# Kernel tuning notes

Hardware: AMD Instinct MI355X
Metric: run time of the kernel (lower is better)

## Reference

```python
import jax, jax.numpy as jnp
import numpy as np

B, N, D, K, NUM_CLASSES = 8, 2048, 256, 8, 32
BN_EPS = 1e-5


def l2norm(x):
    return x / jnp.maximum(jnp.linalg.norm(x, axis=-1, keepdims=True), 1e-12)


def mlp2(x, W1, b1, W2, b2):
    # get_mlp([3, 32, D]): Linear -> ReLU -> Linear -> ReLU
    return jax.nn.relu(jax.nn.relu(x @ W1 + b1) @ W2 + b2)


def bn(x, g, b):
    # training-mode BatchNorm1d over all edges (flattened leading dims)
    ax = tuple(range(x.ndim - 1))
    m = jnp.mean(x, axis=ax, keepdims=True)
    v = jnp.var(x, axis=ax, keepdims=True)
    return (x - m) * jax.lax.rsqrt(v + BN_EPS) * g + b


def setup_inputs() -> dict:
    key = jax.random.key(0)
    ks = jax.random.split(key, 24)
    p = lambda i, shape: jax.random.normal(ks[i], shape, jnp.float32) * 0.05
    class_table = p(0, (NUM_CLASSES, D)).at[0].set(0.0)  # padding_idx=0
    return dict(
        class_idx=jax.random.randint(ks[1], (B, N), 0, NUM_CLASSES),
        colors=jax.random.uniform(ks[2], (B, N, 3), jnp.float32),
        positions=jax.random.normal(ks[3], (B, N, 3), jnp.float32),
        class_table=class_table,
        pos_W1=p(4, (3, 32)), pos_b1=p(5, (32,)),
        pos_W2=p(6, (32, D)), pos_b2=p(7, (D,)),
        col_W1=p(8, (3, 32)), col_b1=p(9, (32,)),
        col_W2=p(10, (32, D)), col_b2=p(11, (D,)),
        merge_W=p(12, (3 * D, D)), merge_b=p(13, (D,)),
        g_W1=p(14, (2 * D, D)), g_b1=p(15, (D,)),
        g_g1=jnp.ones((D,), jnp.float32), g_be1=jnp.zeros((D,), jnp.float32),
        g_W2=p(16, (D, D)), g_b2=p(17, (D,)),
        g_g2=jnp.ones((D,), jnp.float32), g_be2=jnp.zeros((D,), jnp.float32),
        lin_W1=p(18, (D, D)), lin_b1=p(19, (D,)),
        lin_W2=p(20, (D, D)), lin_b2=p(21, (D,)),
    )


def reference(class_idx, colors, positions, class_table,
              pos_W1, pos_b1, pos_W2, pos_b2,
              col_W1, col_b1, col_W2, col_b2,
              merge_W, merge_b,
              g_W1, g_b1, g_g1, g_be1, g_W2, g_b2, g_g2, g_be2,
              lin_W1, lin_b1, lin_W2, lin_b2):
    # --- per-object feature embeddings, each L2-normalized ---
    ce = l2norm(class_table[class_idx])                                   # [B,N,D]
    col = l2norm(mlp2(colors, col_W1, col_b1, col_W2, col_b2))            # [B,N,D]
    pos = l2norm(mlp2(positions, pos_W1, pos_b1, pos_W2, pos_b2))         # [B,N,D]
    x = jax.nn.relu(jnp.concatenate([ce, col, pos], -1) @ merge_W + merge_b)  # [B,N,D]
    # --- dynamic kNN in feature space, per sample (self edge included) ---
    sq = jnp.sum(x * x, -1)                                               # [B,N]
    d = sq[:, :, None] + sq[:, None, :] - 2.0 * jnp.einsum('bid,bjd->bij', x, x)
    _, idx = jax.lax.top_k(-jax.lax.stop_gradient(d), K)                  # [B,N,K]
    xj = jax.vmap(lambda e, i: e[i])(x, idx)                              # [B,N,K,D]
    xi = jnp.broadcast_to(x[:, :, None, :], xj.shape)
    e = jnp.concatenate([xi, xj - xi], -1)                                # [B,N,K,2D]
    # --- edge MLP [2D,D,D] with BN, max aggregation over neighbors ---
    h = bn(jax.nn.relu(e @ g_W1 + g_b1), g_g1, g_be1)
    h = bn(jax.nn.relu(h @ g_W2 + g_b2), g_g2, g_be2)
    node = jnp.max(h, axis=2)                                             # [B,N,D]
    pooled = jnp.max(node, axis=1)                                        # global_max_pool -> [B,D]
    out = jax.nn.relu(jax.nn.relu(pooled @ lin_W1 + lin_b1) @ lin_W2 + lin_b2)
    return l2norm(out)
```

## Files before the change

### kernel.cpp

```cpp
#include <hip/hip_runtime.h>
#include <math.h>

#define BB 8
#define NN 2048
#define DD 256
#define KNN 8
#define NPTS (BB*NN)
#define NEDGE (NPTS*KNN)
#define BN_EPS 1e-5f
#define NSH 64
#define PSH 32

#define OFF_X      0
#define OFF_FEAT   (OFF_X + NPTS*DD)
#define OFF_STATS  (OFF_FEAT + NPTS*3*DD)
#define OFF_PMAXS  (OFF_STATS + NSH*1024)
#define OFF_SQ     (OFF_PMAXS + PSH*BB*DD)
#define OFF_PMINS  (OFF_SQ + NPTS)
#define OFF_IDX    (OFF_PMINS + PSH*BB*DD)
#define OFF_U      (OFF_IDX + NEDGE)
#define OFF_V      (OFF_U + NPTS*DD)
#define OFF_W2BF   (OFF_V + NPTS*DD)
#define OFF_BIASP  (OFF_W2BF + 32768)
#define OFF_XHI    (OFF_BIASP + DD)
#define OFF_XLO    (OFF_XHI + NPTS*DD/2)
#define OFF_MWH    (OFF_XLO + NPTS*DD/2)
#define OFF_MWL    (OFF_MWH + 98304)
#define OFF_WUH    (OFF_MWL + 98304)
#define OFF_WUL    (OFF_WUH + 32768)
#define OFF_WBH    (OFF_WUL + 32768)
#define OFF_WBL    (OFF_WBH + 32768)

typedef __attribute__((ext_vector_type(8))) short bf16x8;
typedef __attribute__((ext_vector_type(4))) float f32x4;

__device__ __forceinline__ unsigned short f2bf(float f) {
  unsigned int u = __float_as_uint(f);
  u += 0x7FFF + ((u >> 16) & 1);
  return (unsigned short)(u >> 16);
}
__device__ __forceinline__ float bf2f(unsigned short h) {
  return __uint_as_float((unsigned int)h << 16);
}

__global__ __launch_bounds__(256) void featurize(
    const int* __restrict__ cls, const float* __restrict__ colors, const float* __restrict__ positions,
    const float* __restrict__ ctab,
    const float* __restrict__ pW1, const float* __restrict__ pb1, const float* __restrict__ pW2, const float* __restrict__ pb2,
    const float* __restrict__ cW1, const float* __restrict__ cb1, const float* __restrict__ cW2, const float* __restrict__ cb2,
    unsigned short* __restrict__ feathi, unsigned short* __restrict__ featlo)
{
  __shared__ float wbuf[4][64];
  int tid = threadIdx.x;
  int wv = tid >> 6, lane = tid & 63;
  int p = blockIdx.x*4 + wv;
  if (lane < 32) {
    float c0 = colors[p*3+0], c1 = colors[p*3+1], c2 = colors[p*3+2];
    wbuf[wv][lane] = fmaxf(c0*cW1[lane] + c1*cW1[32+lane] + c2*cW1[64+lane] + cb1[lane], 0.f);
  } else {
    int l = lane - 32;
    float q0 = positions[p*3+0], q1 = positions[p*3+1], q2 = positions[p*3+2];
    wbuf[wv][32+l] = fmaxf(q0*pW1[l] + q1*pW1[32+l] + q2*pW1[64+l] + pb1[l], 0.f);
  }
  __syncthreads();
  int c = lane*4;
  float4 ce4 = *(const float4*)&ctab[(size_t)cls[p]*DD + c];
  float4 col4 = *(const float4*)&cb2[c];
  float4 pos4 = *(const float4*)&pb2[c];
  #pragma unroll
  for (int k = 0; k < 32; k++) {
    float ch = wbuf[wv][k], ph = wbuf[wv][32+k];
    float4 cw = *(const float4*)&cW2[k*DD + c];
    float4 pw = *(const float4*)&pW2[k*DD + c];
    col4.x += ch*cw.x; col4.y += ch*cw.y; col4.z += ch*cw.z; col4.w += ch*cw.w;
    pos4.x += ph*pw.x; pos4.y += ph*pw.y; pos4.z += ph*pw.z; pos4.w += ph*pw.w;
  }
  col4.x = fmaxf(col4.x, 0.f); col4.y = fmaxf(col4.y, 0.f);
  col4.z = fmaxf(col4.z, 0.f); col4.w = fmaxf(col4.w, 0.f);
  pos4.x = fmaxf(pos4.x, 0.f); pos4.y = fmaxf(pos4.y, 0.f);
  pos4.z = fmaxf(pos4.z, 0.f); pos4.w = fmaxf(pos4.w, 0.f);
  float sce  = ce4.x*ce4.x + ce4.y*ce4.y + ce4.z*ce4.z + ce4.w*ce4.w;
  float scol = col4.x*col4.x + col4.y*col4.y + col4.z*col4.z + col4.w*col4.w;
  float spos = pos4.x*pos4.x + pos4.y*pos4.y + pos4.z*pos4.z + pos4.w*pos4.w;
  #pragma unroll
  for (int m = 1; m <= 32; m <<= 1) {
    sce  += __shfl_xor(sce,  m, 64);
    scol += __shfl_xor(scol, m, 64);
    spos += __shfl_xor(spos, m, 64);
  }
  float ice = 1.f / fmaxf(sqrtf(sce),  1e-12f);
  float icl = 1.f / fmaxf(sqrtf(scol), 1e-12f);
  float ips = 1.f / fmaxf(sqrtf(spos), 1e-12f);
  float o[3][4] = {
    {ce4.x*ice,  ce4.y*ice,  ce4.z*ice,  ce4.w*ice},
    {col4.x*icl, col4.y*icl, col4.z*icl, col4.w*icl},
    {pos4.x*ips, pos4.y*ips, pos4.z*ips, pos4.w*ips}
  };
  #pragma unroll
  for (int sgm = 0; sgm < 3; sgm++) {
    unsigned short h[4], l[4];
    #pragma unroll
    for (int cc = 0; cc < 4; cc++) {
      h[cc] = f2bf(o[sgm][cc]);
      l[cc] = f2bf(o[sgm][cc] - bf2f(h[cc]));
    }
    size_t off = (size_t)p*768 + sgm*256 + c;
    *(uint2*)&feathi[off] = make_uint2((unsigned)h[0] | ((unsigned)h[1] << 16),
                                       (unsigned)h[2] | ((unsigned)h[3] << 16));
    *(uint2*)&featlo[off] = make_uint2((unsigned)l[0] | ((unsigned)l[1] << 16),
                                       (unsigned)l[2] | ((unsigned)l[3] << 16));
  }
}

__global__ __launch_bounds__(256) void prep_mw(const float* __restrict__ mW,
    unsigned short* __restrict__ mwh, unsigned short* __restrict__ mwl)
{
  int k = blockIdx.x;
  int n = threadIdx.x;
  float wgt = mW[(size_t)k*DD + n];
  unsigned short h = f2bf(wgt);
  mwh[(size_t)n*768 + k] = h;
  mwl[(size_t)n*768 + k] = f2bf(wgt - bf2f(h));
}

__global__ __launch_bounds__(256) void prep_uvw(const float* __restrict__ gW1,
    unsigned short* __restrict__ Wuh, unsigned short* __restrict__ Wul,
    unsigned short* __restrict__ Wbh, unsigned short* __restrict__ Wbl)
{
  int k = blockIdx.x;
  int n = threadIdx.x;
  float t = gW1[(size_t)k*DD + n];
  float b = gW1[(size_t)(k + DD)*DD + n];
  float wu = t - b;
  unsigned short uh = f2bf(wu), bh = f2bf(b);
  Wuh[(size_t)n*DD + k] = uh;
  Wul[(size_t)n*DD + k] = f2bf(wu - bf2f(uh));
  Wbh[(size_t)n*DD + k] = bh;
  Wbl[(size_t)n*DD + k] = f2bf(b - bf2f(bh));
}

__global__ __launch_bounds__(256) void gemm768(
    const unsigned short* __restrict__ feathi, const unsigned short* __restrict__ featlo,
    const unsigned short* __restrict__ mwh, const unsigned short* __restrict__ mwl,
    const float* __restrict__ mb,
    float* __restrict__ x, float* __restrict__ sqo,
    unsigned short* __restrict__ xhi, unsigned short* __restrict__ xlo)
{
  __shared__ float wSh[128*18];
  __shared__ float wSl[128*18];
  int tid = threadIdx.x;
  int w = tid >> 6, lane = tid & 63;
  int m = lane & 15, quad = lane >> 4;
  int rowbase = blockIdx.x * 64;
  int colbase = blockIdx.y * 128;
  size_t aoff = (size_t)(rowbase + w*16 + m)*768;
  int srow = tid >> 1;
  int sseg = (tid & 1) * 2;
  f32x4 acc[8];
  #pragma unroll
  for (int t = 0; t < 8; t++) acc[t] = (f32x4){0.f, 0.f, 0.f, 0.f};
  #pragma unroll 1
  for (int c = 0; c < 24; c++) {
    int k0 = c*32 + quad*8;
    bf16x8 ah = *(const bf16x8*)(feathi + aoff + k0);
    bf16x8 al = *(const bf16x8*)(featlo + aoff + k0);
    const float* wrh = (const float*)(mwh + (size_t)(colbase + srow)*768 + c*32);
    const float* wrl = (const float*)(mwl + (size_t)(colbase + srow)*768 + c*32);
    float4 wh0 = *(const float4*)(wrh + sseg*4);
    float4 wh1 = *(const float4*)(wrh + (sseg+1)*4);
    float4 wl0 = *(const float4*)(wrl + sseg*4);
    float4 wl1 = *(const float4*)(wrl + (sseg+1)*4);
    __syncthreads();
    *(float4*)&wSh[srow*18 + sseg*4]     = wh0;
    *(float4*)&wSh[srow*18 + (sseg+1)*4] = wh1;
    *(float4*)&wSl[srow*18 + sseg*4]     = wl0;
    *(float4*)&wSl[srow*18 + (sseg+1)*4] = wl1;
    __syncthreads();
    #pragma unroll
    for (int nt = 0; nt < 8; nt++) {
      bf16x8 bh = *(const bf16x8*)&wSh[(nt*16 + m)*18 + quad*4];
      bf16x8 bl = *(const bf16x8*)&wSl[(nt*16 + m)*18 + quad*4];
      acc[nt] = __builtin_amdgcn_mfma_f32_16x16x32_bf16(ah, bh, acc[nt], 0, 0, 0);
      acc[nt] = __builtin_amdgcn_mfma_f32_16x16x32_bf16(ah, bl, acc[nt], 0, 0, 0);
      acc[nt] = __builtin_amdgcn_mfma_f32_16x16x32_bf16(al, bh, acc[nt], 0, 0, 0);
    }
  }
  float sqp[4] = {0.f, 0.f, 0.f, 0.f};
  #pragma unroll
  for (int nt = 0; nt < 8; nt++) {
    int col = colbase + nt*16 + m;
    float bp = mb[col];
    #pragma unroll
    for (int r = 0; r < 4; r++) {
      float o = fmaxf(acc[nt][r] + bp, 0.f);
      int row = rowbase + w*16 + quad*4 + r;
      x[(size_t)row*DD + col] = o;
      unsigned short h = f2bf(o);
      xhi[(size_t)row*DD + col] = h;
      xlo[(size_t)row*DD + col] = f2bf(o - bf2f(h));
      sqp[r] += o*o;
    }
  }
  #pragma unroll
  for (int r = 0; r < 4; r++) {
    #pragma unroll
    for (int mm = 1; mm <= 8; mm <<= 1) sqp[r] += __shfl_xor(sqp[r], mm, 64);
  }
  if (m == 0) {
    #pragma unroll
    for (int r = 0; r < 4; r++)
      atomicAdd(&sqo[rowbase + w*16 + quad*4 + r], sqp[r]);
  }
}

__global__ __launch_bounds__(256) void gemmuv(
    const unsigned short* __restrict__ xhi, const unsigned short* __restrict__ xlo,
    const unsigned short* __restrict__ Wuh, const unsigned short* __restrict__ Wul,
    const unsigned short* __restrict__ Wbh, const unsigned short* __restrict__ Wbl,
    float* __restrict__ U, float* __restrict__ V)
{
  __shared__ float wSh[128*18];
  __shared__ float wSl[128*18];
  int tid = threadIdx.x;
  int w = tid >> 6, lane = tid & 63;
  int m = lane & 15, quad = lane >> 4;
  int rowbase = blockIdx.x * 64;
  int uv = blockIdx.y >> 1;
  int colbase = (blockIdx.y & 1) * 128;
  const unsigned short* Wh = uv ? Wbh : Wuh;
  const unsigned short* Wl = uv ? Wbl : Wul;
  float* Out = uv ? V : U;
  size_t aoff = (size_t)(rowbase + w*16 + m)*DD;
  int srow = tid >> 1;
  int sseg = (tid & 1) * 2;
  f32x4 acc[8];
  #pragma unroll
  for (int t = 0; t < 8; t++) acc[t] = (f32x4){0.f, 0.f, 0.f, 0.f};
  #pragma unroll 1
  for (int c = 0; c < 8; c++) {
    int k0 = c*32 + quad*8;
    bf16x8 ah = *(const bf16x8*)(xhi + aoff + k0);
    bf16x8 al = *(const bf16x8*)(xlo + aoff + k0);
    const float* wrh = (const float*)(Wh + (size_t)(colbase + srow)*DD + c*32);
    const float* wrl = (const float*)(Wl + (size_t)(colbase + srow)*DD + c*32);
    float4 wh0 = *(const float4*)(wrh + sseg*4);
    float4 wh1 = *(const float4*)(wrh + (sseg+1)*4);
    float4 wl0 = *(const float4*)(wrl + sseg*4);
    float4 wl1 = *(const float4*)(wrl + (sseg+1)*4);
    __syncthreads();
    *(float4*)&wSh[srow*18 + sseg*4]     = wh0;
    *(float4*)&wSh[srow*18 + (sseg+1)*4] = wh1;
    *(float4*)&wSl[srow*18 + sseg*4]     = wl0;
    *(float4*)&wSl[srow*18 + (sseg+1)*4] = wl1;
    __syncthreads();
    #pragma unroll
    for (int nt = 0; nt < 8; nt++) {
      bf16x8 bh = *(const bf16x8*)&wSh[(nt*16 + m)*18 + quad*4];
      bf16x8 bl = *(const bf16x8*)&wSl[(nt*16 + m)*18 + quad*4];
      acc[nt] = __builtin_amdgcn_mfma_f32_16x16x32_bf16(ah, bh, acc[nt], 0, 0, 0);
      acc[nt] = __builtin_amdgcn_mfma_f32_16x16x32_bf16(ah, bl, acc[nt], 0, 0, 0);
      acc[nt] = __builtin_amdgcn_mfma_f32_16x16x32_bf16(al, bh, acc[nt], 0, 0, 0);
    }
  }
  #pragma unroll
  for (int nt = 0; nt < 8; nt++) {
    int col = colbase + nt*16 + m;
    #pragma unroll
    for (int r = 0; r < 4; r++) {
      int row = rowbase + w*16 + quad*4 + r;
      Out[(size_t)row*DD + col] = acc[nt][r];
    }
  }
}

__global__ __launch_bounds__(256) void knnk(
    const unsigned short* __restrict__ xhi, const unsigned short* __restrict__ xlo,
    const float* __restrict__ sq,
    float* __restrict__ pdg, int* __restrict__ pjg)
{
  __shared__ float smem[4736];
  float* jh = smem;
  float* jl = smem + 2304;
  float (*dt)[65] = (float(*)[65])smem;
  float* sqI = smem + 4608;
  float* sqJ = smem + 4672;
  int tid = threadIdx.x;
  int q  = blockIdx.x & 3;
  int it = (blockIdx.x >> 2) & 31;
  int bb = blockIdx.x >> 7;
  int ibase = it * 64;
  const unsigned short* xhb = xhi + (size_t)bb*NN*DD;
  const unsigned short* xlb = xlo + (size_t)bb*NN*DD;
  const float* sqb = sq + (size_t)bb*NN;
  int w = tid >> 6, lane = tid & 63;
  int m = lane & 15, quad = lane >> 4;
  int selrow = tid & 63, selseg = tid >> 6;
  size_t aoff = (size_t)(ibase + w*16 + m)*DD;
  int srow = tid >> 2;
  int sseg = tid & 3;
  bf16x8 ahr[8], alr[8];
  #pragma unroll
  for (int c = 0; c < 8; c++) {
    int k0 = c*32 + quad*8;
    ahr[c] = *(const bf16x8*)(xhb + aoff + k0);
    alr[c] = *(const bf16x8*)(xlb + aoff + k0);
  }
  float bd[8]; int bj[8];
  #pragma unroll
  for (int s = 0; s < 8; s++) { bd[s] = 3.4e38f; bj[s] = 0; }
  if (tid < 64) sqI[tid] = sqb[ibase + tid];
  #pragma unroll 1
  for (int jt = 0; jt < 8; jt++) {
    int jbase = q*512 + jt*64;
    if (tid < 64) sqJ[tid] = sqb[jbase + tid];
    f32x4 acc[4];
    #pragma unroll
    for (int t = 0; t < 4; t++) acc[t] = (f32x4){0.f, 0.f, 0.f, 0.f};
    #pragma unroll
    for (int c2 = 0; c2 < 4; c2++) {
      size_t gb = (size_t)(jbase + srow)*DD + c2*64;
      float4 h0 = *(const float4*)((const float*)(xhb + gb) + sseg*4);
      float4 h1 = *(const float4*)((const float*)(xhb + gb) + (sseg+4)*4);
      float4 l0 = *(const float4*)((const float*)(xlb + gb) + sseg*4);
      float4 l1 = *(const float4*)((const float*)(xlb + gb) + (sseg+4)*4);
      __syncthreads();
      *(float4*)&jh[srow*36 + sseg*4]     = h0;
      *(float4*)&jh[srow*36 + (sseg+4)*4] = h1;
      *(float4*)&jl[srow*36 + sseg*4]     = l0;
      *(float4*)&jl[srow*36 + (sseg+4)*4] = l1;
      __syncthreads();
      #pragma unroll
      for (int kk = 0; kk < 2; kk++) {
        bf16x8 ah = ahr[c2*2 + kk];
        bf16x8 al = alr[c2*2 + kk];
        int lofs = kk*16 + quad*4;
        #pragma unroll
        for (int nt = 0; nt < 4; nt++) {
          int r = nt*16 + m;
          bf16x8 bh = *(const bf16x8*)&jh[r*36 + lofs];
          bf16x8 bl = *(const bf16x8*)&jl[r*36 + lofs];
          acc[nt] = __builtin_amdgcn_mfma_f32_16x16x32_bf16(ah, bh, acc[nt], 0, 0, 0);
          acc[nt] = __builtin_amdgcn_mfma_f32_16x16x32_bf16(ah, bl, acc[nt], 0, 0, 0);
          acc[nt] = __builtin_amdgcn_mfma_f32_16x16x32_bf16(al, bh, acc[nt], 0, 0, 0);
        }
      }
    }
    __syncthreads();
    #pragma unroll
    for (int nt = 0; nt < 4; nt++) {
      int col = nt*16 + m;
      float sj = sqJ[col];
      #pragma unroll
      for (int r = 0; r < 4; r++) {
        int rowl = w*16 + quad*4 + r;
        dt[rowl][col] = sqI[rowl] + sj - 2.f*acc[nt][r];
      }
    }
    __syncthreads();
    int cb = selseg*16;
    #pragma unroll
    for (int s = 0; s < 16; s++) {
      float dv = dt[selrow][cb + s];
      if (dv < bd[7]) {
        bd[7] = dv; bj[7] = jbase + cb + s;
        #pragma unroll
        for (int t = 7; t >= 1; t--) {
          if (bd[t] < bd[t-1]) {
            float td = bd[t]; bd[t] = bd[t-1]; bd[t-1] = td;
            int   tj = bj[t]; bj[t] = bj[t-1]; bj[t-1] = tj;
          }
        }
      }
    }
  }
  __syncthreads();
  float* pdl = &smem[0];
  int*   pjl = (int*)&smem[2048];
  #pragma unroll
  for (int s = 0; s < 8; s++) {
    pdl[tid*8 + s] = bd[s];
    pjl[tid*8 + s] = bj[s];
  }
  __syncthreads();
  if (tid < 64) {
    float md[8]; int mj[8];
    #pragma unroll
    for (int s = 0; s < 8; s++) { md[s] = 3.4e38f; mj[s] = 0; }
    #pragma unroll 1
    for (int g = 0; g < 4; g++) {
      int base = (g*64 + tid)*8;
      #pragma unroll
      for (int s = 0; s < 8; s++) {
        float dv = pdl[base + s];
        if (dv < md[7]) {
          md[7] = dv; mj[7] = pjl[base + s];
          #pragma unroll
          for (int t = 7; t >= 1; t--) {
            if (md[t] < md[t-1]) {
              float td = md[t]; md[t] = md[t-1]; md[t-1] = td;
              int   tj = mj[t]; mj[t] = mj[t-1]; mj[t-1] = tj;
            }
          }
        }
      }
    }
    size_t gbase = ((size_t)(bb*NN + ibase + tid))*32 + (size_t)q*8;
    #pragma unroll
    for (int s = 0; s < 8; s++) {
      pdg[gbase + s] = md[s];
      pjg[gbase + s] = bb*NN + mj[s];
    }
  }
}

__global__ __launch_bounds__(256) void knnmerge(const float* __restrict__ pdg, const int* __restrict__ pjg,
                                                int* __restrict__ idxg)
{
  int p = blockIdx.x*256 + threadIdx.x;
  float md[8]; int mj[8];
  #pragma unroll
  for (int s = 0; s < 8; s++) { md[s] = 3.4e38f; mj[s] = 0; }
  size_t base = (size_t)p*32;
  #pragma unroll 1
  for (int s = 0; s < 32; s++) {
    float dv = pdg[base + s];
    if (dv < md[7]) {
      md[7] = dv; mj[7] = pjg[base + s];
      #pragma unroll
      for (int t = 7; t >= 1; t--) {
        if (md[t] < md[t-1]) {
          float td = md[t]; md[t] = md[t-1]; md[t-1] = td;
          int   tj = mj[t]; mj[t] = mj[t-1]; mj[t-1] = tj;
        }
      }
    }
  }
  #pragma unroll
  for (int s = 0; s < 8; s++) idxg[(size_t)p*8 + s] = mj[s];
}

__global__ __launch_bounds__(256) void bn1stats(const float* __restrict__ u, const float* __restrict__ v,
    const int* __restrict__ idxg, const float* __restrict__ b1, float* __restrict__ stats)
{
  __shared__ int jL[128];
  int c = threadIdx.x;
  int n0 = blockIdx.x * 16;
  if (c < 128) jL[c] = idxg[(size_t)n0*8 + c];
  __syncthreads();
  float b1c = b1[c];
  float s = 0.f, s2 = 0.f;
  #pragma unroll 1
  for (int n = 0; n < 16; n++) {
    float uc = u[(size_t)(n0 + n)*DD + c];
    #pragma unroll
    for (int e = 0; e < 8; e++) {
      int j = jL[n*8 + e];
      float h = fmaxf(uc + v[(size_t)j*DD + c] + b1c, 0.f);
      s += h; s2 += h*h;
    }
  }
  int row = blockIdx.x & (NSH - 1);
  atomicAdd(&stats[row*1024 + c], s);
  atomicAdd(&stats[row*1024 + 256 + c], s2);
}

__global__ __launch_bounds__(256) void prep2(const float* __restrict__ stats, const float* __restrict__ g1,
    const float* __restrict__ be1, const float* __restrict__ gW2, const float* __restrict__ gb2,
    unsigned short* __restrict__ w2bf, float* __restrict__ biasp)
{
  __shared__ float s1L[256], t1L[256];
  int tid = threadIdx.x;
  const float inv = 1.f / (float)NEDGE;
  float sm = 0.f, sq2 = 0.f;
  #pragma unroll 1
  for (int r = 0; r < NSH; r++) {
    sm  += stats[r*1024 + tid];
    sq2 += stats[r*1024 + 256 + tid];
  }
  float m = sm * inv;
  float var = sq2*inv - m*m;
  float s1 = g1[tid] / sqrtf(var + BN_EPS);
  s1L[tid] = s1; t1L[tid] = be1[tid] - m*s1;
  __syncthreads();
  float bacc = gb2[tid];
  for (int k = 0; k < DD; k++) {
    float w = gW2[k*DD + tid];
    w2bf[(size_t)tid*DD + k] = f2bf(s1L[k]*w);
    bacc += t1L[k]*w;
  }
  biasp[tid] = bacc;
}

__global__ __launch_bounds__(256) void edgek(
// ... 106 lines not shown
}

__global__ __launch_bounds__(256) void finalk(const float* __restrict__ pmaxs, const float* __restrict__ pmins,
    const float* __restrict__ stats, const float* __restrict__ g2, const float* __restrict__ be2,
    const float* __restrict__ W1, const float* __restrict__ b1,
    const float* __restrict__ W2, const float* __restrict__ b2,
    float* __restrict__ out)
{
  __shared__ float pl[256];
  __shared__ float hl[256];
  __shared__ float red[4];
  int c = threadIdx.x;
  int b = blockIdx.x;
  const float inv = 1.f / (float)NEDGE;
  float sm = 0.f, sq2 = 0.f;
  #pragma unroll 1
  for (int r = 0; r < NSH; r++) {
    sm  += stats[r*1024 + 512 + c];
    sq2 += stats[r*1024 + 768 + c];
  }
  float m = sm * inv;
  float var = sq2*inv - m*m;
  float s2 = g2[c] / sqrtf(var + BN_EPS);
  float t2 = be2[c] - m*s2;
  float mx = -3.4e38f, mn = 3.4e38f;
  #pragma unroll 1
  for (int s = 0; s < PSH; s++) {
    mx = fmaxf(mx, pmaxs[((size_t)s*BB + b)*DD + c]);
    mn = fminf(mn, pmins[((size_t)s*BB + b)*DD + c]);
  }
  pl[c] = (s2 >= 0.f) ? s2*mx + t2 : s2*mn + t2;
  __syncthreads();
  float h = b1[c];
  #pragma unroll 4
  for (int k = 0; k < 256; k++) h += pl[k]*W1[k*256 + c];
  hl[c] = fmaxf(h, 0.f);
  __syncthreads();
  float o = b2[c];
  #pragma unroll 4
  for (int k = 0; k < 256; k++) o += hl[k]*W2[k*256 + c];
  o = fmaxf(o, 0.f);
  float s = o*o;
  #pragma unroll
  for (int mm = 1; mm <= 32; mm <<= 1) s += __shfl_xor(s, mm, 64);
  if ((c & 63) == 0) red[c >> 6] = s;
  __syncthreads();
  float tot = red[0] + red[1] + red[2] + red[3];
  out[b*256 + c] = o / fmaxf(sqrtf(tot), 1e-12f);
}

extern "C" void kernel_launch(void* const* d_in, const int* in_sizes, int n_in,
                              void* d_out, int out_size, void* d_ws, size_t ws_size,
                              hipStream_t stream) {
  (void)in_sizes; (void)n_in; (void)out_size; (void)ws_size;
  const int*   cls       = (const int*)  d_in[0];
  const float* colors    = (const float*)d_in[1];
  const float* positions = (const float*)d_in[2];
  const float* ctab      = (const float*)d_in[3];
  const float* pW1 = (const float*)d_in[4];
  const float* pb1 = (const float*)d_in[5];
  const float* pW2 = (const float*)d_in[6];
  const float* pb2 = (const float*)d_in[7];
  const float* cW1 = (const float*)d_in[8];
  const float* cb1 = (const float*)d_in[9];
  const float* cW2 = (const float*)d_in[10];
  const float* cb2 = (const float*)d_in[11];
  const float* mW  = (const float*)d_in[12];
  const float* mb  = (const float*)d_in[13];
  const float* gW1 = (const float*)d_in[14];
  const float* gb1 = (const float*)d_in[15];
  const float* gg1 = (const float*)d_in[16];
  const float* gbe1= (const float*)d_in[17];
  const float* gW2 = (const float*)d_in[18];
  const float* gb2 = (const float*)d_in[19];
  const float* gg2 = (const float*)d_in[20];
  const float* gbe2= (const float*)d_in[21];
  const float* lW1 = (const float*)d_in[22];
  const float* lb1 = (const float*)d_in[23];
  const float* lW2 = (const float*)d_in[24];
  const float* lb2 = (const float*)d_in[25];
  float* out = (float*)d_out;

  float* wsf   = (float*)d_ws;
  float* x     = wsf + OFF_X;
  unsigned short* feathi = (unsigned short*)(wsf + OFF_FEAT);
  unsigned short* featlo = feathi + (size_t)NPTS*768;
  float* sq    = wsf + OFF_SQ;
  int*   idxg  = (int*)(wsf + OFF_IDX);
  float* u     = wsf + OFF_U;
  float* v     = wsf + OFF_V;
  unsigned short* w2bf = (unsigned short*)(wsf + OFF_W2BF);
  float* biasp = wsf + OFF_BIASP;
  unsigned short* xhi = (unsigned short*)(wsf + OFF_XHI);
  unsigned short* xlo = (unsigned short*)(wsf + OFF_XLO);
  unsigned short* mwh = (unsigned short*)(wsf + OFF_MWH);
  unsigned short* mwl = (unsigned short*)(wsf + OFF_MWL);
  unsigned short* Wuh = (unsigned short*)(wsf + OFF_WUH);
  unsigned short* Wul = (unsigned short*)(wsf + OFF_WUL);
  unsigned short* Wbh = (unsigned short*)(wsf + OFF_WBH);
  unsigned short* Wbl = (unsigned short*)(wsf + OFF_WBL);
  float* stats = wsf + OFF_STATS;
  float* pmaxs = wsf + OFF_PMAXS;
  float* pmins = wsf + OFF_PMINS;
  float* pdg   = wsf + OFF_FEAT;
  int*   pjg   = (int*)(wsf + OFF_FEAT + (size_t)NPTS*32);

  hipMemsetAsync(stats, 0, (NSH*1024 + PSH*BB*DD + NPTS)*sizeof(float), stream);
  hipMemsetAsync(pmins, 0x7f, PSH*BB*DD*sizeof(float), stream);

  featurize<<<NPTS/4, 256, 0, stream>>>(cls, colors, positions, ctab,
                                        pW1, pb1, pW2, pb2, cW1, cb1, cW2, cb2, feathi, featlo);
  prep_mw<<<768, 256, 0, stream>>>(mW, mwh, mwl);
  prep_uvw<<<DD, 256, 0, stream>>>(gW1, Wuh, Wul, Wbh, Wbl);
  gemm768<<<dim3(NPTS/64, 2), 256, 0, stream>>>(feathi, featlo, mwh, mwl, mb, x, sq, xhi, xlo);
  knnk<<<BB*32*4, 256, 0, stream>>>(xhi, xlo, sq, pdg, pjg);
  knnmerge<<<NPTS/256, 256, 0, stream>>>(pdg, pjg, idxg);
  gemmuv<<<dim3(NPTS/64, 4), 256, 0, stream>>>(xhi, xlo, Wuh, Wul, Wbh, Wbl, u, v);
  bn1stats<<<NPTS/16, 256, 0, stream>>>(u, v, idxg, gb1, stats);
  prep2<<<1, 256, 0, stream>>>(stats, gg1, gbe1, gW2, gb2, w2bf, biasp);
  edgek<<<dim3(NEDGE/64, 2), 256, 0, stream>>>(u, v, idxg, gb1, w2bf, biasp, pmaxs, pmins, stats);
  finalk<<<BB, 256, 0, stream>>>(pmaxs, pmins, stats, gg2, gbe2, lW1, lb1, lW2, lb2, out);
}
```

Measured before the change: 538.4 us.

## Merge prep kernels and co-schedule kNN with U/V GEMM in one launch

Folds featurize, prep_mw and prep_uvw into a single launch that branches on block index. It also interleaves the kNN distance blocks with the U/V projection GEMM blocks in one kernel (even blocks do kNN, odd blocks do GEMM), so the two independent workloads can overlap on the device. The unused fp32 x write in gemm768 is dropped, cutting global store traffic. In exchange the merged kernels carry the register and LDS footprint of the heavier branch, which may lower occupancy.

```diff
diff --git a/kernel.cpp b/kernel.cpp
--- a/kernel.cpp
+++ b/kernel.cpp
@@ -43,107 +43,106 @@
   return __uint_as_float((unsigned int)h << 16);
 }
 
-__global__ __launch_bounds__(256) void featurize(
+__global__ __launch_bounds__(256) void prepk(
     const int* __restrict__ cls, const float* __restrict__ colors, const float* __restrict__ positions,
     const float* __restrict__ ctab,
     const float* __restrict__ pW1, const float* __restrict__ pb1, const float* __restrict__ pW2, const float* __restrict__ pb2,
     const float* __restrict__ cW1, const float* __restrict__ cb1, const float* __restrict__ cW2, const float* __restrict__ cb2,
-    unsigned short* __restrict__ feathi, unsigned short* __restrict__ featlo)
-{
-  __shared__ float wbuf[4][64];
-  int tid = threadIdx.x;
-  int wv = tid >> 6, lane = tid & 63;
-  int p = blockIdx.x*4 + wv;
-  if (lane < 32) {
-    float c0 = colors[p*3+0], c1 = colors[p*3+1], c2 = colors[p*3+2];
-    wbuf[wv][lane] = fmaxf(c0*cW1[lane] + c1*cW1[32+lane] + c2*cW1[64+lane] + cb1[lane], 0.f);
-  } else {
-    int l = lane - 32;
-    float q0 = positions[p*3+0], q1 = positions[p*3+1], q2 = positions[p*3+2];
-    wbuf[wv][32+l] = fmaxf(q0*pW1[l] + q1*pW1[32+l] + q2*pW1[64+l] + pb1[l], 0.f);
-  }
-  __syncthreads();
-  int c = lane*4;
-  float4 ce4 = *(const float4*)&ctab[(size_t)cls[p]*DD + c];
-  float4 col4 = *(const float4*)&cb2[c];
-  float4 pos4 = *(const float4*)&pb2[c];
-  #pragma unroll
-  for (int k = 0; k < 32; k++) {
-    float ch = wbuf[wv][k], ph = wbuf[wv][32+k];
-    float4 cw = *(const float4*)&cW2[k*DD + c];
-    float4 pw = *(const float4*)&pW2[k*DD + c];
-    col4.x += ch*cw.x; col4.y += ch*cw.y; col4.z += ch*cw.z; col4.w += ch*cw.w;
-    pos4.x += ph*pw.x; pos4.y += ph*pw.y; pos4.z += ph*pw.z; pos4.w += ph*pw.w;
-  }
-  col4.x = fmaxf(col4.x, 0.f); col4.y = fmaxf(col4.y, 0.f);
-  col4.z = fmaxf(col4.z, 0.f); col4.w = fmaxf(col4.w, 0.f);
-  pos4.x = fmaxf(pos4.x, 0.f); pos4.y = fmaxf(pos4.y, 0.f);
-  pos4.z = fmaxf(pos4.z, 0.f); pos4.w = fmaxf(pos4.w, 0.f);
-  float sce  = ce4.x*ce4.x + ce4.y*ce4.y + ce4.z*ce4.z + ce4.w*ce4.w;
-  float scol = col4.x*col4.x + col4.y*col4.y + col4.z*col4.z + col4.w*col4.w;
-  float spos = pos4.x*pos4.x + pos4.y*pos4.y + pos4.z*pos4.z + pos4.w*pos4.w;
-  #pragma unroll
-  for (int m = 1; m <= 32; m <<= 1) {
-    sce  += __shfl_xor(sce,  m, 64);
-    scol += __shfl_xor(scol, m, 64);
-    spos += __shfl_xor(spos, m, 64);
-  }
-  float ice = 1.f / fmaxf(sqrtf(sce),  1e-12f);
-  float icl = 1.f / fmaxf(sqrtf(scol), 1e-12f);
-  float ips = 1.f / fmaxf(sqrtf(spos), 1e-12f);
-  float o[3][4] = {
-    {ce4.x*ice,  ce4.y*ice,  ce4.z*ice,  ce4.w*ice},
-    {col4.x*icl, col4.y*icl, col4.z*icl, col4.w*icl},
-    {pos4.x*ips, pos4.y*ips, pos4.z*ips, pos4.w*ips}
-  };
-  #pragma unroll
-  for (int sgm = 0; sgm < 3; sgm++) {
-    unsigned short h[4], l[4];
-    #pragma unroll
-    for (int cc = 0; cc < 4; cc++) {
-      h[cc] = f2bf(o[sgm][cc]);
-      l[cc] = f2bf(o[sgm][cc] - bf2f(h[cc]));
-    }
-    size_t off = (size_t)p*768 + sgm*256 + c;
-    *(uint2*)&feathi[off] = make_uint2((unsigned)h[0] | ((unsigned)h[1] << 16),
-                                       (unsigned)h[2] | ((unsigned)h[3] << 16));
-    *(uint2*)&featlo[off] = make_uint2((unsigned)l[0] | ((unsigned)l[1] << 16),
-                                       (unsigned)l[2] | ((unsigned)l[3] << 16));
-  }
-}
-
-__global__ __launch_bounds__(256) void prep_mw(const float* __restrict__ mW,
-    unsigned short* __restrict__ mwh, unsigned short* __restrict__ mwl)
-{
-  int k = blockIdx.x;
-  int n = threadIdx.x;
-  float wgt = mW[(size_t)k*DD + n];
-  unsigned short h = f2bf(wgt);
-  mwh[(size_t)n*768 + k] = h;
-  mwl[(size_t)n*768 + k] = f2bf(wgt - bf2f(h));
-}
-
-__global__ __launch_bounds__(256) void prep_uvw(const float* __restrict__ gW1,
+    unsigned short* __restrict__ feathi, unsigned short* __restrict__ featlo,
+    const float* __restrict__ mW,
+    unsigned short* __restrict__ mwh, unsigned short* __restrict__ mwl,
+    const float* __restrict__ gW1,
     unsigned short* __restrict__ Wuh, unsigned short* __restrict__ Wul,
     unsigned short* __restrict__ Wbh, unsigned short* __restrict__ Wbl)
 {
-  int k = blockIdx.x;
-  int n = threadIdx.x;
-  float t = gW1[(size_t)k*DD + n];
-  float b = gW1[(size_t)(k + DD)*DD + n];
-  float wu = t - b;
-  unsigned short uh = f2bf(wu), bh = f2bf(b);
-  Wuh[(size_t)n*DD + k] = uh;
-  Wul[(size_t)n*DD + k] = f2bf(wu - bf2f(uh));
-  Wbh[(size_t)n*DD + k] = bh;
-  Wbl[(size_t)n*DD + k] = f2bf(b - bf2f(bh));
+  __shared__ float wbuf[4][64];
+  int bx = blockIdx.x;
+  int tid = threadIdx.x;
+  if (bx < 4096) {
+    int wv = tid >> 6, lane = tid & 63;
+    int p = bx*4 + wv;
+    if (lane < 32) {
+      float c0 = colors[p*3+0], c1 = colors[p*3+1], c2 = colors[p*3+2];
+      wbuf[wv][lane] = fmaxf(c0*cW1[lane] + c1*cW1[32+lane] + c2*cW1[64+lane] + cb1[lane], 0.f);
+    } else {
+      int l = lane - 32;
+      float q0 = positions[p*3+0], q1 = positions[p*3+1], q2 = positions[p*3+2];
+      wbuf[wv][32+l] = fmaxf(q0*pW1[l] + q1*pW1[32+l] + q2*pW1[64+l] + pb1[l], 0.f);
+    }
+    __syncthreads();
+    int c = lane*4;
+    float4 ce4 = *(const float4*)&ctab[(size_t)cls[p]*DD + c];
+    float4 col4 = *(const float4*)&cb2[c];
+    float4 pos4 = *(const float4*)&pb2[c];
+    #pragma unroll
+    for (int k = 0; k < 32; k++) {
+      float ch = wbuf[wv][k], ph = wbuf[wv][32+k];
+      float4 cw = *(const float4*)&cW2[k*DD + c];
+      float4 pw = *(const float4*)&pW2[k*DD + c];
+      col4.x += ch*cw.x; col4.y += ch*cw.y; col4.z += ch*cw.z; col4.w += ch*cw.w;
+      pos4.x += ph*pw.x; pos4.y += ph*pw.y; pos4.z += ph*pw.z; pos4.w += ph*pw.w;
+    }
+    col4.x = fmaxf(col4.x, 0.f); col4.y = fmaxf(col4.y, 0.f);
+    col4.z = fmaxf(col4.z, 0.f); col4.w = fmaxf(col4.w, 0.f);
+    pos4.x = fmaxf(pos4.x, 0.f); pos4.y = fmaxf(pos4.y, 0.f);
+    pos4.z = fmaxf(pos4.z, 0.f); pos4.w = fmaxf(pos4.w, 0.f);
+    float sce  = ce4.x*ce4.x + ce4.y*ce4.y + ce4.z*ce4.z + ce4.w*ce4.w;
+    float scol = col4.x*col4.x + col4.y*col4.y + col4.z*col4.z + col4.w*col4.w;
+    float spos = pos4.x*pos4.x + pos4.y*pos4.y + pos4.z*pos4.z + pos4.w*pos4.w;
+    #pragma unroll
+    for (int m = 1; m <= 32; m <<= 1) {
+      sce  += __shfl_xor(sce,  m, 64);
+      scol += __shfl_xor(scol, m, 64);
+      spos += __shfl_xor(spos, m, 64);
+    }
+    float ice = 1.f / fmaxf(sqrtf(sce),  1e-12f);
+    float icl = 1.f / fmaxf(sqrtf(scol), 1e-12f);
+    float ips = 1.f / fmaxf(sqrtf(spos), 1e-12f);
+    float o[3][4] = {
+      {ce4.x*ice,  ce4.y*ice,  ce4.z*ice,  ce4.w*ice},
+      {col4.x*icl, col4.y*icl, col4.z*icl, col4.w*icl},
+      {pos4.x*ips, pos4.y*ips, pos4.z*ips, pos4.w*ips}
+    };
+    #pragma unroll
+    for (int sgm = 0; sgm < 3; sgm++) {
+      unsigned short h[4], l[4];
+      #pragma unroll
+      for (int cc = 0; cc < 4; cc++) {
+        h[cc] = f2bf(o[sgm][cc]);
+        l[cc] = f2bf(o[sgm][cc] - bf2f(h[cc]));
+      }
+      size_t off = (size_t)p*768 + sgm*256 + c;
+      *(uint2*)&feathi[off] = make_uint2((unsigned)h[0] | ((unsigned)h[1] << 16),
+                                         (unsigned)h[2] | ((unsigned)h[3] << 16));
+      *(uint2*)&featlo[off] = make_uint2((unsigned)l[0] | ((unsigned)l[1] << 16),
+                                         (unsigned)l[2] | ((unsigned)l[3] << 16));
+    }
+  } else if (bx < 4096 + 768) {
+    int k = bx - 4096;
+    int n = tid;
+    float wgt = mW[(size_t)k*DD + n];
+    unsigned short h = f2bf(wgt);
+    mwh[(size_t)n*768 + k] = h;
+    mwl[(size_t)n*768 + k] = f2bf(wgt - bf2f(h));
+  } else {
+    int k = bx - (4096 + 768);
+    int n = tid;
+    float t = gW1[(size_t)k*DD + n];
+    float b = gW1[(size_t)(k + DD)*DD + n];
+    float wu = t - b;
+    unsigned short uh = f2bf(wu), bh = f2bf(b);
+    Wuh[(size_t)n*DD + k] = uh;
+    Wul[(size_t)n*DD + k] = f2bf(wu - bf2f(uh));
+    Wbh[(size_t)n*DD + k] = bh;
+    Wbl[(size_t)n*DD + k] = f2bf(b - bf2f(bh));
+  }
 }
 
 __global__ __launch_bounds__(256) void gemm768(
     const unsigned short* __restrict__ feathi, const unsigned short* __restrict__ featlo,
     const unsigned short* __restrict__ mwh, const unsigned short* __restrict__ mwl,
     const float* __restrict__ mb,
-    float* __restrict__ x, float* __restrict__ sqo,
+    float* __restrict__ sqo,
     unsigned short* __restrict__ xhi, unsigned short* __restrict__ xlo)
 {
   __shared__ float wSh[128*18];
@@ -194,7 +193,6 @@
     for (int r = 0; r < 4; r++) {
       float o = fmaxf(acc[nt][r] + bp, 0.f);
       int row = rowbase + w*16 + quad*4 + r;
-      x[(size_t)row*DD + col] = o;
       unsigned short h = f2bf(o);
       xhi[(size_t)row*DD + col] = h;
       xlo[(size_t)row*DD + col] = f2bf(o - bf2f(h));
@@ -213,202 +211,201 @@
   }
 }
 
-__global__ __launch_bounds__(256) void gemmuv(
+__global__ __launch_bounds__(256) void knnuv(
     const unsigned short* __restrict__ xhi, const unsigned short* __restrict__ xlo,
+    const float* __restrict__ sq,
+    float* __restrict__ pdg, int* __restrict__ pjg,
     const unsigned short* __restrict__ Wuh, const unsigned short* __restrict__ Wul,
     const unsigned short* __restrict__ Wbh, const unsigned short* __restrict__ Wbl,
     float* __restrict__ U, float* __restrict__ V)
 {
-  __shared__ float wSh[128*18];
-  __shared__ float wSl[128*18];
+  __shared__ float smem[4736];
+  int bx = blockIdx.x;
   int tid = threadIdx.x;
   int w = tid >> 6, lane = tid & 63;
   int m = lane & 15, quad = lane >> 4;
-  int rowbase = blockIdx.x * 64;
-  int uv = blockIdx.y >> 1;
-  int colbase = (blockIdx.y & 1) * 128;
-  const unsigned short* Wh = uv ? Wbh : Wuh;
-  const unsigned short* Wl = uv ? Wbl : Wul;
-  float* Out = uv ? V : U;
-  size_t aoff = (size_t)(rowbase + w*16 + m)*DD;
-  int srow = tid >> 1;
-  int sseg = (tid & 1) * 2;
-  f32x4 acc[8];
-  #pragma unroll
-  for (int t = 0; t < 8; t++) acc[t] = (f32x4){0.f, 0.f, 0.f, 0.f};
-  #pragma unroll 1
-  for (int c = 0; c < 8; c++) {
-    int k0 = c*32 + quad*8;
-    bf16x8 ah = *(const bf16x8*)(xhi + aoff + k0);
-    bf16x8 al = *(const bf16x8*)(xlo + aoff + k0);
-    const float* wrh = (const float*)(Wh + (size_t)(colbase + srow)*DD + c*32);
-    const float* wrl = (const float*)(Wl + (size_t)(colbase + srow)*DD + c*32);
-    float4 wh0 = *(const float4*)(wrh + sseg*4);
-    float4 wh1 = *(const float4*)(wrh + (sseg+1)*4);
-    float4 wl0 = *(const float4*)(wrl + sseg*4);
-    float4 wl1 = *(const float4*)(wrl + (sseg+1)*4);
-    __syncthreads();
-    *(float4*)&wSh[srow*18 + sseg*4]     = wh0;
-    *(float4*)&wSh[srow*18 + (sseg+1)*4] = wh1;
-    *(float4*)&wSl[srow*18 + sseg*4]     = wl0;
-    *(float4*)&wSl[srow*18 + (sseg+1)*4] = wl1;
-    __syncthreads();
-    #pragma unroll
-    for (int nt = 0; nt < 8; nt++) {
-      bf16x8 bh = *(const bf16x8*)&wSh[(nt*16 + m)*18 + quad*4];
-      bf16x8 bl = *(const bf16x8*)&wSl[(nt*16 + m)*18 + quad*4];
-      acc[nt] = __builtin_amdgcn_mfma_f32_16x16x32_bf16(ah, bh, acc[nt], 0, 0, 0);
-      acc[nt] = __builtin_amdgcn_mfma_f32_16x16x32_bf16(ah, bl, acc[nt], 0, 0, 0);
-      acc[nt] = __builtin_amdgcn_mfma_f32_16x16x32_bf16(al, bh, acc[nt], 0, 0, 0);
-    }
-  }
-  #pragma unroll
-  for (int nt = 0; nt < 8; nt++) {
-    int col = colbase + nt*16 + m;
-    #pragma unroll
-    for (int r = 0; r < 4; r++) {
-      int row = rowbase + w*16 + quad*4 + r;
-      Out[(size_t)row*DD + col] = acc[nt][r];
-    }
-  }
-}
-
-__global__ __launch_bounds__(256) void knnk(
-    const unsigned short* __restrict__ xhi, const unsigned short* __restrict__ xlo,
-    const float* __restrict__ sq,
-    float* __restrict__ pdg, int* __restrict__ pjg)
-{
-  __shared__ float smem[4736];
-  float* jh = smem;
-  float* jl = smem + 2304;
-  float (*dt)[65] = (float(*)[65])smem;
-  float* sqI = smem + 4608;
-  float* sqJ = smem + 4672;
-  int tid = threadIdx.x;
-  int q  = blockIdx.x & 3;
-  int it = (blockIdx.x >> 2) & 31;
-  int bb = blockIdx.x >> 7;
-  int ibase = it * 64;
-  const unsigned short* xhb = xhi + (size_t)bb*NN*DD;
-  const unsigned short* xlb = xlo + (size_t)bb*NN*DD;
-  const float* sqb = sq + (size_t)bb*NN;
-  int w = tid >> 6, lane = tid & 63;
-  int m = lane & 15, quad = lane >> 4;
-  int selrow = tid & 63, selseg = tid >> 6;
-  size_t aoff = (size_t)(ibase + w*16 + m)*DD;
-  int srow = tid >> 2;
-  int sseg = tid & 3;
-  bf16x8 ahr[8], alr[8];
-  #pragma unroll
-  for (int c = 0; c < 8; c++) {
-    int k0 = c*32 + quad*8;
-    ahr[c] = *(const bf16x8*)(xhb + aoff + k0);
-    alr[c] = *(const bf16x8*)(xlb + aoff + k0);
-  }
-  float bd[8]; int bj[8];
-  #pragma unroll
-  for (int s = 0; s < 8; s++) { bd[s] = 3.4e38f; bj[s] = 0; }
-  if (tid < 64) sqI[tid] = sqb[ibase + tid];
-  #pragma unroll 1
-  for (int jt = 0; jt < 8; jt++) {
-    int jbase = q*512 + jt*64;
-    if (tid < 64) sqJ[tid] = sqb[jbase + tid];
-    f32x4 acc[4];
-    #pragma unroll
-    for (int t = 0; t < 4; t++) acc[t] = (f32x4){0.f, 0.f, 0.f, 0.f};
-    #pragma unroll
-    for (int c2 = 0; c2 < 4; c2++) {
-      size_t gb = (size_t)(jbase + srow)*DD + c2*64;
-      float4 h0 = *(const float4*)((const float*)(xhb + gb) + sseg*4);
-      float4 h1 = *(const float4*)((const float*)(xhb + gb) + (sseg+4)*4);
-      float4 l0 = *(const float4*)((const float*)(xlb + gb) + sseg*4);
-      float4 l1 = *(const float4*)((const float*)(xlb + gb) + (sseg+4)*4);
-      __syncthreads();
-      *(float4*)&jh[srow*36 + sseg*4]     = h0;
-      *(float4*)&jh[srow*36 + (sseg+4)*4] = h1;
-      *(float4*)&jl[srow*36 + sseg*4]     = l0;
-      *(float4*)&jl[srow*36 + (sseg+4)*4] = l1;
-      __syncthreads();
-      #pragma unroll
-      for (int kk = 0; kk < 2; kk++) {
-        bf16x8 ah = ahr[c2*2 + kk];
-        bf16x8 al = alr[c2*2 + kk];
-        int lofs = kk*16 + quad*4;
+  if ((bx & 1) == 0) {
+    int kid = bx >> 1;
+    float* jh = smem;
+    float* jl = smem + 2304;
+    float (*dt)[65] = (float(*)[65])smem;
+    float* sqI = smem + 4608;
+    float* sqJ = smem + 4672;
+    int q  = kid & 3;
+    int it = (kid >> 2) & 31;
+    int bb = kid >> 7;
+    int ibase = it * 64;
+    const unsigned short* xhb = xhi + (size_t)bb*NN*DD;
+    const unsigned short* xlb = xlo + (size_t)bb*NN*DD;
+    const float* sqb = sq + (size_t)bb*NN;
+    int selrow = tid & 63, selseg = tid >> 6;
+    size_t aoff = (size_t)(ibase + w*16 + m)*DD;
+    int srow = tid >> 2;
+    int sseg = tid & 3;
+    bf16x8 ahr[8], alr[8];
+    #pragma unroll
+    for (int c = 0; c < 8; c++) {
+      int k0 = c*32 + quad*8;
+      ahr[c] = *(const bf16x8*)(xhb + aoff + k0);
+      alr[c] = *(const bf16x8*)(xlb + aoff + k0);
+    }
+    float bd[8]; int bj[8];
+    #pragma unroll
+    for (int s = 0; s < 8; s++) { bd[s] = 3.4e38f; bj[s] = 0; }
+    if (tid < 64) sqI[tid] = sqb[ibase + tid];
+    #pragma unroll 1
+    for (int jt = 0; jt < 8; jt++) {
+      int jbase = q*512 + jt*64;
+      if (tid < 64) sqJ[tid] = sqb[jbase + tid];
+      f32x4 acc[4];
+      #pragma unroll
+      for (int t = 0; t < 4; t++) acc[t] = (f32x4){0.f, 0.f, 0.f, 0.f};
+      #pragma unroll
+      for (int c2 = 0; c2 < 4; c2++) {
+        size_t gb = (size_t)(jbase + srow)*DD + c2*64;
+        float4 h0 = *(const float4*)((const float*)(xhb + gb) + sseg*4);
+        float4 h1 = *(const float4*)((const float*)(xhb + gb) + (sseg+4)*4);
+        float4 l0 = *(const float4*)((const float*)(xlb + gb) + sseg*4);
+        float4 l1 = *(const float4*)((const float*)(xlb + gb) + (sseg+4)*4);
+        __syncthreads();
+        *(float4*)&jh[srow*36 + sseg*4]     = h0;
+        *(float4*)&jh[srow*36 + (sseg+4)*4] = h1;
+        *(float4*)&jl[srow*36 + sseg*4]     = l0;
+        *(float4*)&jl[srow*36 + (sseg+4)*4] = l1;
+        __syncthreads();
         #pragma unroll
-        for (int nt = 0; nt < 4; nt++) {
-          int r = nt*16 + m;
-          bf16x8 bh = *(const bf16x8*)&jh[r*36 + lofs];
-          bf16x8 bl = *(const bf16x8*)&jl[r*36 + lofs];
-          acc[nt] = __builtin_amdgcn_mfma_f32_16x16x32_bf16(ah, bh, acc[nt], 0, 0, 0);
-          acc[nt] = __builtin_amdgcn_mfma_f32_16x16x32_bf16(ah, bl, acc[nt], 0, 0, 0);
-          acc[nt] = __builtin_amdgcn_mfma_f32_16x16x32_bf16(al, bh, acc[nt], 0, 0, 0);
-        }
-      }
-    }
-    __syncthreads();
-    #pragma unroll
-    for (int nt = 0; nt < 4; nt++) {
-      int col = nt*16 + m;
-      float sj = sqJ[col];
-      #pragma unroll
-      for (int r = 0; r < 4; r++) {
-        int rowl = w*16 + quad*4 + r;
-        dt[rowl][col] = sqI[rowl] + sj - 2.f*acc[nt][r];
-      }
-    }
-    __syncthreads();
-    int cb = selseg*16;
-    #pragma unroll
-    for (int s = 0; s < 16; s++) {
-      float dv = dt[selrow][cb + s];
-      if (dv < bd[7]) {
-        bd[7] = dv; bj[7] = jbase + cb + s;
-        #pragma unroll
-        for (int t = 7; t >= 1; t--) {
-          if (bd[t] < bd[t-1]) {
-            float td = bd[t]; bd[t] = bd[t-1]; bd[t-1] = td;
-            int   tj = bj[t]; bj[t] = bj[t-1]; bj[t-1] = tj;
+        for (int kk = 0; kk < 2; kk++) {
+          bf16x8 ah = ahr[c2*2 + kk];
+          bf16x8 al = alr[c2*2 + kk];
+          int lofs = kk*16 + quad*4;
+          #pragma unroll
+          for (int nt = 0; nt < 4; nt++) {
+            int r = nt*16 + m;
+            bf16x8 bh = *(const bf16x8*)&jh[r*36 + lofs];
+            bf16x8 bl = *(const bf16x8*)&jl[r*36 + lofs];
+            acc[nt] = __builtin_amdgcn_mfma_f32_16x16x32_bf16(ah, bh, acc[nt], 0, 0, 0);
+            acc[nt] = __builtin_amdgcn_mfma_f32_16x16x32_bf16(ah, bl, acc[nt], 0, 0, 0);
+            acc[nt] = __builtin_amdgcn_mfma_f32_16x16x32_bf16(al, bh, acc[nt], 0, 0, 0);
           }
         }
       }
-    }
-  }
-  __syncthreads();
-  float* pdl = &smem[0];
-  int*   pjl = (int*)&smem[2048];
-  #pragma unroll
-  for (int s = 0; s < 8; s++) {
-    pdl[tid*8 + s] = bd[s];
-    pjl[tid*8 + s] = bj[s];
-  }
-  __syncthreads();
-  if (tid < 64) {
-    float md[8]; int mj[8];
-    #pragma unroll
-    for (int s = 0; s < 8; s++) { md[s] = 3.4e38f; mj[s] = 0; }
-    #pragma unroll 1
-    for (int g = 0; g < 4; g++) {
-      int base = (g*64 + tid)*8;
-      #pragma unroll
-      for (int s = 0; s < 8; s++) {
-        float dv = pdl[base + s];
-        if (dv < md[7]) {
-          md[7] = dv; mj[7] = pjl[base + s];
+      __syncthreads();
+      #pragma unroll
+      for (int nt = 0; nt < 4; nt++) {
+        int col = nt*16 + m;
+        float sj = sqJ[col];
+        #pragma unroll
+        for (int r = 0; r < 4; r++) {
+          int rowl = w*16 + quad*4 + r;
+          dt[rowl][col] = sqI[rowl] + sj - 2.f*acc[nt][r];
+        }
+      }
+      __syncthreads();
+      int cb = selseg*16;
+      #pragma unroll
+      for (int s = 0; s < 16; s++) {
+        float dv = dt[selrow][cb + s];
+        if (dv < bd[7]) {
+          bd[7] = dv; bj[7] = jbase + cb + s;
           #pragma unroll
           for (int t = 7; t >= 1; t--) {
-            if (md[t] < md[t-1]) {
-              float td = md[t]; md[t] = md[t-1]; md[t-1] = td;
-              int   tj = mj[t]; mj[t] = mj[t-1]; mj[t-1] = tj;
+            if (bd[t] < bd[t-1]) {
+              float td = bd[t]; bd[t] = bd[t-1]; bd[t-1] = td;
+              int   tj = bj[t]; bj[t] = bj[t-1]; bj[t-1] = tj;
             }
           }
         }
       }
     }
-    size_t gbase = ((size_t)(bb*NN + ibase + tid))*32 + (size_t)q*8;
+    __syncthreads();
+    float* pdl = &smem[0];
+    int*   pjl = (int*)&smem[2048];
     #pragma unroll
     for (int s = 0; s < 8; s++) {
-      pdg[gbase + s] = md[s];
-      pjg[gbase + s] = bb*NN + mj[s];
+      pdl[tid*8 + s] = bd[s];
+      pjl[tid*8 + s] = bj[s];
+    }
+    __syncthreads();
+    if (tid < 64) {
+      float md[8]; int mj[8];
+      #pragma unroll
+      for (int s = 0; s < 8; s++) { md[s] = 3.4e38f; mj[s] = 0; }
+      #pragma unroll 1
+      for (int g = 0; g < 4; g++) {
+        int base = (g*64 + tid)*8;
+        #pragma unroll
+        for (int s = 0; s < 8; s++) {
+          float dv = pdl[base + s];
+          if (dv < md[7]) {
+            md[7] = dv; mj[7] = pjl[base + s];
+            #pragma unroll
+            for (int t = 7; t >= 1; t--) {
+              if (md[t] < md[t-1]) {
+                float td = md[t]; md[t] = md[t-1]; md[t-1] = td;
+                int   tj = mj[t]; mj[t] = mj[t-1]; mj[t-1] = tj;
+              }
+            }
+          }
+        }
+      }
+      size_t gbase = ((size_t)(bb*NN + ibase + tid))*32 + (size_t)q*8;
+      #pragma unroll
+      for (int s = 0; s < 8; s++) {
+        pdg[gbase + s] = md[s];
+        pjg[gbase + s] = bb*NN + mj[s];
+      }
+    }
+  } else {
+    int gid = bx >> 1;
+    float* wSh = smem;
+    float* wSl = smem + 2304;
+    int rowbase = (gid & 255) * 64;
+    int yy = gid >> 8;
+    int uv = yy >> 1;
+    int colbase = (yy & 1) * 128;
+    const unsigned short* Wh = uv ? Wbh : Wuh;
+    const unsigned short* Wl = uv ? Wbl : Wul;
+    float* Out = uv ? V : U;
+    size_t aoff = (size_t)(rowbase + w*16 + m)*DD;
+    int srow = tid >> 1;
+    int sseg = (tid & 1) * 2;
+    f32x4 acc[8];
+    #pragma unroll
+    for (int t = 0; t < 8; t++) acc[t] = (f32x4){0.f, 0.f, 0.f, 0.f};
+    #pragma unroll 1
+    for (int c = 0; c < 8; c++) {
+      int k0 = c*32 + quad*8;
+      bf16x8 ah = *(const bf16x8*)(xhi + aoff + k0);
+      bf16x8 al = *(const bf16x8*)(xlo + aoff + k0);
+      const float* wrh = (const float*)(Wh + (size_t)(colbase + srow)*DD + c*32);
+      const float* wrl = (const float*)(Wl + (size_t)(colbase + srow)*DD + c*32);
+      float4 wh0 = *(const float4*)(wrh + sseg*4);
+      float4 wh1 = *(const float4*)(wrh + (sseg+1)*4);
+      float4 wl0 = *(const float4*)(wrl + sseg*4);
+      float4 wl1 = *(const float4*)(wrl + (sseg+1)*4);
+      __syncthreads();
+      *(float4*)&wSh[srow*18 + sseg*4]     = wh0;
+      *(float4*)&wSh[srow*18 + (sseg+1)*4] = wh1;
+      *(float4*)&wSl[srow*18 + sseg*4]     = wl0;
+      *(float4*)&wSl[srow*18 + (sseg+1)*4] = wl1;
+      __syncthreads();
+      #pragma unroll
+      for (int nt = 0; nt < 8; nt++) {
+        bf16x8 bh = *(const bf16x8*)&wSh[(nt*16 + m)*18 + quad*4];
+        bf16x8 bl = *(const bf16x8*)&wSl[(nt*16 + m)*18 + quad*4];
+        acc[nt] = __builtin_amdgcn_mfma_f32_16x16x32_bf16(ah, bh, acc[nt], 0, 0, 0);
+        acc[nt] = __builtin_amdgcn_mfma_f32_16x16x32_bf16(ah, bl, acc[nt], 0, 0, 0);
+        acc[nt] = __builtin_amdgcn_mfma_f32_16x16x32_bf16(al, bh, acc[nt], 0, 0, 0);
+      }
+    }
+    #pragma unroll
+    for (int nt = 0; nt < 8; nt++) {
+      int col = colbase + nt*16 + m;
+      #pragma unroll
+      for (int r = 0; r < 4; r++) {
+        int row = rowbase + w*16 + quad*4 + r;
+        Out[(size_t)row*DD + col] = acc[nt][r];
+      }
     }
   }
 }
@@ -681,7 +678,6 @@
   float* out = (float*)d_out;
 
   float* wsf   = (float*)d_ws;
-  float* x     = wsf + OFF_X;
   unsigned short* feathi = (unsigned short*)(wsf + OFF_FEAT);
   unsigned short* featlo = feathi + (size_t)NPTS*768;
   float* sq    = wsf + OFF_SQ;
@@ -707,14 +703,13 @@
   hipMemsetAsync(stats, 0, (NSH*1024 + PSH*BB*DD + NPTS)*sizeof(float), stream);
   hipMemsetAsync(pmins, 0x7f, PSH*BB*DD*sizeof(float), stream);
 
-  featurize<<<NPTS/4, 256, 0, stream>>>(cls, colors, positions, ctab,
-                                        pW1, pb1, pW2, pb2, cW1, cb1, cW2, cb2, feathi, featlo);
-  prep_mw<<<768, 256, 0, stream>>>(mW, mwh, mwl);
-  prep_uvw<<<DD, 256, 0, stream>>>(gW1, Wuh, Wul, Wbh, Wbl);
-  gemm768<<<dim3(NPTS/64, 2), 256, 0, stream>>>(feathi, featlo, mwh, mwl, mb, x, sq, xhi, xlo);
-  knnk<<<BB*32*4, 256, 0, stream>>>(xhi, xlo, sq, pdg, pjg);
+  prepk<<<4096 + 768 + 256, 256, 0, stream>>>(cls, colors, positions, ctab,
+                                              pW1, pb1, pW2, pb2, cW1, cb1, cW2, cb2,
+                                              feathi, featlo, mW, mwh, mwl,
+                                              gW1, Wuh, Wul, Wbh, Wbl);
+  gemm768<<<dim3(NPTS/64, 2), 256, 0, stream>>>(feathi, featlo, mwh, mwl, mb, sq, xhi, xlo);
+  knnuv<<<2048, 256, 0, stream>>>(xhi, xlo, sq, pdg, pjg, Wuh, Wul, Wbh, Wbl, u, v);
   knnmerge<<<NPTS/256, 256, 0, stream>>>(pdg, pjg, idxg);
-  gemmuv<<<dim3(NPTS/64, 4), 256, 0, stream>>>(xhi, xlo, Wuh, Wul, Wbh, Wbl, u, v);
   bn1stats<<<NPTS/16, 256, 0, stream>>>(u, v, idxg, gb1, stats);
   prep2<<<1, 256, 0, stream>>>(stats, gg1, gbe1, gW2, gb2, w2bf, biasp);
   edgek<<<dim3(NEDGE/64, 2), 256, 0, stream>>>(u, v, idxg, gb1, w2bf, biasp, pmaxs, pmins, stats);
```

Result: slower. 605.9 us (+12.5%).
